# Performance work log

Hardware: AMD Instinct MI355X
Metric: run time of the kernel (lower is better)

## Reference

```python
import jax, jax.numpy as jnp
import numpy as np

DIM = 1024
N_HEADS = 16
HEAD_DIM = DIM // N_HEADS


def setup_inputs() -> dict:
    key = jax.random.key(0)
    ks = jax.random.split(key, 7)
    B, S = 2, 2048
    scale = 0.02
    return {
        "q": jax.random.normal(ks[0], (B, S, DIM), dtype=jnp.float32),
        "k": jax.random.normal(ks[1], (B, S, DIM), dtype=jnp.float32),
        "v": jax.random.normal(ks[2], (B, S, DIM), dtype=jnp.float32),
        # torch nn.Linear weights are [out_features, in_features]; y = x @ W.T
        "wq": jax.random.normal(ks[3], (DIM, DIM), dtype=jnp.float32) * scale,
        "wk": jax.random.normal(ks[4], (DIM, DIM), dtype=jnp.float32) * scale,
        "wv": jax.random.normal(ks[5], (DIM, DIM), dtype=jnp.float32) * scale,
        "wo": jax.random.normal(ks[6], (DIM, DIM), dtype=jnp.float32) * scale,
    }


def reference(q, k, v, wq, wk, wv, wo):
    B, S, _ = q.shape
    H, D = N_HEADS, HEAD_DIM
    # projections (torch Linear: x @ W.T), reshape to [B, H, S, D]
    xq = (q @ wq.T).reshape(B, S, H, D).transpose(0, 2, 1, 3)
    xk = (k @ wk.T).reshape(B, S, H, D).transpose(0, 2, 1, 3)
    xv = (v @ wv.T).reshape(B, S, H, D).transpose(0, 2, 1, 3)
    # scaled dot-product attention with causal mask
    scores = jnp.einsum("bhqd,bhkd->bhqk", xq, xk) / jnp.sqrt(jnp.float32(D))
    causal = jnp.tril(jnp.ones((S, S), dtype=bool))
    scores = jnp.where(causal, scores, -jnp.inf)
    attn = jax.nn.softmax(scores.astype(jnp.float32), axis=-1).astype(xq.dtype)
    # dropout prob = 0.0 (eval-mode / deterministic reference)
    out = jnp.einsum("bhqk,bhkd->bhqd", attn, xv)
    out = out.transpose(0, 2, 1, 3).reshape(B, S, H * D)
    return out @ wo.T
```

## Files before the change

kernel.cpp:

```cpp
#include <hip/hip_runtime.h>
#include <hip/hip_bf16.h>
#include <stdint.h>


typedef short s16x8 __attribute__((ext_vector_type(8)));
typedef float f32x4 __attribute__((ext_vector_type(4)));

#define MFMA_BF16 __builtin_amdgcn_mfma_f32_16x16x32_bf16

static __device__ __forceinline__ unsigned short f2bf(float f) {
    union { float f; unsigned u; } x{f};
    unsigned r = x.u + 0x7fff + ((x.u >> 16) & 1);
    return (unsigned short)(r >> 16);
}
static __device__ __forceinline__ unsigned pk2h(float a, float b) {
    __hip_bfloat162 h = __float22bfloat162_rn(float2{a, b});
    return *(unsigned*)&h;
}

static __device__ __forceinline__ void ald16(unsigned short* lds, const unsigned short* g) {
    __builtin_amdgcn_global_load_lds(
        (const __attribute__((address_space(1))) unsigned int*)g,
        (__attribute__((address_space(3))) unsigned int*)lds, 16, 0, 0);
}

#define QSCL 0.18033688f

__global__ __launch_bounds__(256) void convert_all_kernel(
        const float* __restrict__ q, const float* __restrict__ k,
        const float* __restrict__ v,
        const float* __restrict__ wq, const float* __restrict__ wk,
        const float* __restrict__ wv, const float* __restrict__ wo,
        unsigned short* __restrict__ dst) {
    const size_t idx = ((size_t)blockIdx.x * 256 + threadIdx.x) * 8;
    const int region = (int)(idx >> 22);
    const float* src;
    size_t off;
    if (region == 0)      { src = q; off = idx; }
    else if (region == 1) { src = k; off = idx & 4194303; }
    else if (region == 2) { src = v; off = idx & 4194303; }
    else {
        const int wsel = (int)((idx >> 20) & 3);
        src = wsel == 0 ? wq : wsel == 1 ? wk : wsel == 2 ? wv : wo;
        off = idx & 1048575;
    }
    const float4* p = (const float4*)(src + off);
    float4 a = p[0], b = p[1];
    uint4 u;
    u.x = pk2h(a.x, a.y); u.y = pk2h(a.z, a.w);
    u.z = pk2h(b.x, b.y); u.w = pk2h(b.z, b.w);
    *(uint4*)(dst + idx) = u;
}

__global__ __launch_bounds__(256) void wconvert_kernel(
        const float* __restrict__ wq, const float* __restrict__ wk,
        const float* __restrict__ wv, const float* __restrict__ wo,
        unsigned short* __restrict__ Wb) {
    const size_t idx = ((size_t)blockIdx.x * 256 + threadIdx.x) * 8;
    const int region = (int)(idx >> 20);
    const size_t off = idx & 1048575;
    const float* src = region == 0 ? wq : region == 1 ? wk : region == 2 ? wv : wo;
    const float4* p = (const float4*)(src + off);
    float4 a = p[0], b = p[1];
    uint4 u;
    u.x = pk2h(a.x, a.y); u.y = pk2h(a.z, a.w);
    u.z = pk2h(b.x, b.y); u.w = pk2h(b.z, b.w);
    *(uint4*)(Wb + idx) = u;
}

__global__ __launch_bounds__(256) void proj3b_kernel(
        const unsigned short* __restrict__ Qb, const unsigned short* __restrict__ Kb,
        const unsigned short* __restrict__ Vb, const unsigned short* __restrict__ Wb,
        unsigned short* __restrict__ Xq, unsigned short* __restrict__ Xk,
        unsigned short* __restrict__ Xvt) {
    constexpr int Kd = 1024;
    __shared__ union {
        struct { unsigned short A[128 * 32]; unsigned short B[128 * 32]; } s;
        unsigned short T[4 * 64 * 68];
    } sm;

    const int z = blockIdx.z;
    const unsigned short* A  = z == 0 ? Qb : z == 1 ? Kb : Vb;
    const unsigned short* Bw = Wb + (size_t)z * 1048576;

    const int t = threadIdx.x;
    const int m0 = blockIdx.x * 128, n0 = blockIdx.y * 128;
    const int w = t >> 6, lane = t & 63, fr = lane & 15, g = lane >> 4;
    const int wm = (w >> 1) * 64, wn = (w & 1) * 64;
    const int brow = t >> 2;
    const int cB = (t & 3) ^ ((t >> 3) & 3);
    const int sB = g ^ ((fr >> 1) & 3);

    f32x4 acc[4][4] = {};

    for (int k0 = 0; k0 < Kd; k0 += 32) {
        ald16(sm.s.A + (size_t)w * 512,        A  + (size_t)(m0 + brow) * Kd + k0 + cB * 8);
        ald16(sm.s.A + 2048 + (size_t)w * 512, A  + (size_t)(m0 + 64 + brow) * Kd + k0 + cB * 8);
        ald16(sm.s.B + (size_t)w * 512,        Bw + (size_t)(n0 + brow) * Kd + k0 + cB * 8);
        ald16(sm.s.B + 2048 + (size_t)w * 512, Bw + (size_t)(n0 + 64 + brow) * Kd + k0 + cB * 8);
        __syncthreads();

        s16x8 af[4], bfv[4];
#pragma unroll
        for (int mi = 0; mi < 4; ++mi)
            af[mi] = *(const s16x8*)(sm.s.A + (wm + mi * 16 + fr) * 32 + sB * 8);
#pragma unroll
        for (int ni = 0; ni < 4; ++ni)
            bfv[ni] = *(const s16x8*)(sm.s.B + (wn + ni * 16 + fr) * 32 + sB * 8);
#pragma unroll
        for (int mi = 0; mi < 4; ++mi)
#pragma unroll
            for (int ni = 0; ni < 4; ++ni)
                acc[mi][ni] = MFMA_BF16(af[mi], bfv[ni], acc[mi][ni], 0, 0, 0);
        __syncthreads();
    }

    if (z != 2) {
        unsigned short* C = z ? Xk : Xq;
        const float osc = z == 0 ? QSCL : 1.0f;
#pragma unroll
        for (int mi = 0; mi < 4; ++mi)
#pragma unroll
            for (int ni = 0; ni < 4; ++ni)
#pragma unroll
                for (int reg = 0; reg < 4; ++reg)
                    C[(size_t)(m0 + wm + mi * 16 + g * 4 + reg) * 1024 +
                      n0 + wn + ni * 16 + fr] = f2bf(acc[mi][ni][reg] * osc);
    } else {
        unsigned short* T = sm.T + w * (64 * 68);
#pragma unroll
        for (int mi = 0; mi < 4; ++mi)
#pragma unroll
            for (int ni = 0; ni < 4; ++ni) {
                uint2 u;
                u.x = pk2h(acc[mi][ni][0], acc[mi][ni][1]);
                u.y = pk2h(acc[mi][ni][2], acc[mi][ni][3]);
                *(uint2*)(T + (ni * 16 + fr) * 68 + mi * 16 + g * 4) = u;
            }
        __asm__ __volatile__("" ::: "memory");
#pragma unroll
        for (int pass = 0; pass < 8; ++pass) {
            const int row = pass * 8 + (lane >> 3);
            const int chk = lane & 7;
            uint4 d = *(const uint4*)(T + row * 68 + chk * 8);
            *(uint4*)(Xvt + (size_t)(n0 + wn + row) * 4096 + m0 + wm + chk * 8) = d;
        }
    }
}

__global__ __launch_bounds__(256) void proj3_kernel(
        const float* __restrict__ q, const float* __restrict__ k, const float* __restrict__ v,
        const unsigned short* __restrict__ Wb,
        unsigned short* __restrict__ Xq, unsigned short* __restrict__ Xk,
        unsigned short* __restrict__ Xvt) {
    constexpr int Kd = 1024;
    __shared__ unsigned short lsA[128 * 40];
    __shared__ unsigned short lsB[128 * 32];
    __shared__ unsigned short Tls[4 * 64 * 68];

    const int z = blockIdx.z;
    const float* A = z == 0 ? q : z == 1 ? k : v;
    const unsigned short* Bw = Wb + (size_t)z * 1048576;

    const int t = threadIdx.x;
    const int m0 = blockIdx.x * 128, n0 = blockIdx.y * 128;
    const int w = t >> 6, lane = t & 63, fr = lane & 15, g = lane >> 4, fq = g * 8;
    const int wm = (w >> 1) * 64, wn = (w & 1) * 64;
    const int ar = t >> 1, ac = (t & 1) * 16;
    const int brow = t >> 2;
    const int cB = (t & 3) ^ ((t >> 3) & 3);
    const int sB = g ^ ((fr >> 1) & 3);

    f32x4 acc[4][4] = {};

    for (int k0 = 0; k0 < Kd; k0 += 32) {
        ald16(lsB + (size_t)w * 512,        Bw + (size_t)(n0 + brow) * Kd + k0 + cB * 8);
        ald16(lsB + 2048 + (size_t)w * 512, Bw + (size_t)(n0 + 64 + brow) * Kd + k0 + cB * 8);
        {
            const float4* pa = (const float4*)(A + (size_t)(m0 + ar) * Kd + k0 + ac);
            float4 a0 = pa[0], a1 = pa[1], a2 = pa[2], a3 = pa[3];
            uint4 u0, u1;
            u0.x = pk2h(a0.x, a0.y); u0.y = pk2h(a0.z, a0.w);
            u0.z = pk2h(a1.x, a1.y); u0.w = pk2h(a1.z, a1.w);
            u1.x = pk2h(a2.x, a2.y); u1.y = pk2h(a2.z, a2.w);
            u1.z = pk2h(a3.x, a3.y); u1.w = pk2h(a3.z, a3.w);
            *(uint4*)(lsA + ar * 40 + ac)     = u0;
            *(uint4*)(lsA + ar * 40 + ac + 8) = u1;
        }
        __syncthreads();

        s16x8 af[4], bfv[4];
#pragma unroll
        for (int mi = 0; mi < 4; ++mi)
            af[mi] = *(const s16x8*)(lsA + (wm + mi * 16 + fr) * 40 + fq);
#pragma unroll
        for (int ni = 0; ni < 4; ++ni)
            bfv[ni] = *(const s16x8*)(lsB + (wn + ni * 16 + fr) * 32 + sB * 8);
#pragma unroll
        for (int mi = 0; mi < 4; ++mi)
#pragma unroll
            for (int ni = 0; ni < 4; ++ni)
                acc[mi][ni] = MFMA_BF16(af[mi], bfv[ni], acc[mi][ni], 0, 0, 0);
        __syncthreads();
    }

    if (z != 2) {
        unsigned short* C = z ? Xk : Xq;
        const float osc = z == 0 ? QSCL : 1.0f;
#pragma unroll
        for (int mi = 0; mi < 4; ++mi)
#pragma unroll
            for (int ni = 0; ni < 4; ++ni)
#pragma unroll
                for (int reg = 0; reg < 4; ++reg)
                    C[(size_t)(m0 + wm + mi * 16 + g * 4 + reg) * 1024 +
                      n0 + wn + ni * 16 + fr] = f2bf(acc[mi][ni][reg] * osc);
    } else {
        unsigned short* T = Tls + w * (64 * 68);
#pragma unroll
        for (int mi = 0; mi < 4; ++mi)
#pragma unroll
            for (int ni = 0; ni < 4; ++ni) {
                uint2 u;
                u.x = pk2h(acc[mi][ni][0], acc[mi][ni][1]);
                u.y = pk2h(acc[mi][ni][2], acc[mi][ni][3]);
                *(uint2*)(T + (ni * 16 + fr) * 68 + mi * 16 + g * 4) = u;
            }
        __asm__ __volatile__("" ::: "memory");
#pragma unroll
        for (int pass = 0; pass < 8; ++pass) {
            const int row = pass * 8 + (lane >> 3);
            const int chk = lane & 7;
            uint4 d = *(const uint4*)(T + row * 68 + chk * 8);
            *(uint4*)(Xvt + (size_t)(n0 + wn + row) * 4096 + m0 + wm + chk * 8) = d;
        }
    }
}

static __device__ __forceinline__ void slab_tail(
        const f32x4 sf[4], int kt, int qt, int qrow, float& l_part,
        f32x4* oacc, unsigned short* Pw, const s16x8 vf[4][2], int fr, int g) {
    float e[4][4];
    const bool diag = (kt == qt);
#pragma unroll
    for (int m16 = 0; m16 < 4; ++m16)
#pragma unroll
        for (int r = 0; r < 4; ++r) {
            float x = sf[m16][r];
            if (diag) {
                const int keyg = kt * 64 + m16 * 16 + g * 4 + r;
                x = (keyg <= qrow) ? x : -1e30f;
            }
            const float ee = exp2f(x);
            e[m16][r] = ee;
            l_part += ee;
        }
#pragma unroll
    for (int m16 = 0; m16 < 4; ++m16) {
        uint2 u;
        u.x = pk2h(e[m16][0], e[m16][1]);
        u.y = pk2h(e[m16][2], e[m16][3]);
        const int ch = 2 * m16 + (g >> 1);
        *(uint2*)(Pw + fr * 64 + ((ch ^ (fr & 7)) * 8) + (g & 1) * 4) = u;
    }
    __asm__ __volatile__("" ::: "memory");
    s16x8 pf0 = *(const s16x8*)(Pw + fr * 64 + ((g ^ (fr & 7)) * 8));
    s16x8 pf1 = *(const s16x8*)(Pw + fr * 64 + (((4 + g) ^ (fr & 7)) * 8));
#pragma unroll
    for (int m16 = 0; m16 < 4; ++m16) {
        oacc[m16] = MFMA_BF16(vf[m16][0], pf0, oacc[m16], 0, 0, 0);
        oacc[m16] = MFMA_BF16(vf[m16][1], pf1, oacc[m16], 0, 0, 0);
    }
    __asm__ __volatile__("" ::: "memory");
}

__global__ __launch_bounds__(256, 2) void flash_attn_kernel(
        const unsigned short* __restrict__ Xq, const unsigned short* __restrict__ Xk,
        const unsigned short* __restrict__ Xvt, unsigned short* __restrict__ Oa) {
    __shared__ unsigned short Kls[64 * 64];
    __shared__ unsigned short Vls[64 * 64];
    __shared__ unsigned short Pls[4][16 * 64];

    const int t = threadIdx.x;
    const int bh = blockIdx.x;
    const int j = blockIdx.y;
    const int b = bh >> 4, h = bh & 15;
    const size_t rbase = (size_t)b * 2048;
    const int cbase = h * 64;

    const int w = t >> 6, lane = t & 63, fr = lane & 15, g = lane >> 4, fq = g * 8;
    const int qtH = 31 - j, qtL = j;
    const int qrowH = qtH * 64 + w * 16 + fr;
    const int qrowL = qtL * 64 + w * 16 + fr;

    const unsigned short* qpH = Xq + (rbase + qrowH) * 1024 + cbase;
    s16x8 qfH0 = *(const s16x8*)(qpH + fq);
    s16x8 qfH1 = *(const s16x8*)(qpH + 32 + fq);
    const unsigned short* qpL = Xq + (rbase + qrowL) * 1024 + cbase;
    s16x8 qfL0 = *(const s16x8*)(qpL + fq);
    s16x8 qfL1 = *(const s16x8*)(qpL + 32 + fq);

    float lH = 0.f, lL = 0.f;
    f32x4 oH[4] = {}, oL[4] = {};

    const int r0 = w * 16 + (lane >> 3), r1 = r0 + 8;
    const int s8 = lane & 7;
    const int c0 = s8 ^ (r0 & 7), c1 = s8 ^ (r1 & 7);
    const unsigned short* kbase = Xk + rbase * 1024 + cbase;
    const size_t vrow0 = (size_t)(cbase + r0) * 4096 + rbase + c0 * 8;
    const size_t vrow1 = (size_t)(cbase + r1) * 4096 + rbase + c1 * 8;

    uint4 kA, kB, vA, vB;
    kA = *(const uint4*)(kbase + (size_t)r0 * 1024 + c0 * 8);
    kB = *(const uint4*)(kbase + (size_t)r1 * 1024 + c1 * 8);
    vA = *(const uint4*)(Xvt + vrow0);
    vB = *(const uint4*)(Xvt + vrow1);

    for (int kt = 0; kt <= qtH; ++kt) {
        *(uint4*)(Kls + (w * 16) * 64 + lane * 8)     = kA;
        *(uint4*)(Kls + (w * 16 + 8) * 64 + lane * 8) = kB;
        *(uint4*)(Vls + (w * 16) * 64 + lane * 8)     = vA;
        *(uint4*)(Vls + (w * 16 + 8) * 64 + lane * 8) = vB;
        __syncthreads();

        if (kt < qtH) {
            const unsigned short* ks = kbase + (size_t)(kt + 1) * 65536;
            kA = *(const uint4*)(ks + (size_t)r0 * 1024 + c0 * 8);
            kB = *(const uint4*)(ks + (size_t)r1 * 1024 + c1 * 8);
            vA = *(const uint4*)(Xvt + vrow0 + (size_t)(kt + 1) * 64);
            vB = *(const uint4*)(Xvt + vrow1 + (size_t)(kt + 1) * 64);
        }

        const bool doL = (kt <= qtL);

        s16x8 kf[4][2], vf[4][2];
#pragma unroll
        for (int m16 = 0; m16 < 4; ++m16) {
            const int rr = m16 * 16 + fr;
            kf[m16][0] = *(const s16x8*)(Kls + rr * 64 + ((g ^ (fr & 7)) * 8));
            kf[m16][1] = *(const s16x8*)(Kls + rr * 64 + (((4 + g) ^ (fr & 7)) * 8));
            vf[m16][0] = *(const s16x8*)(Vls + rr * 64 + ((g ^ (fr & 7)) * 8));
            vf[m16][1] = *(const s16x8*)(Vls + rr * 64 + (((4 + g) ^ (fr & 7)) * 8));
        }

        f32x4 sH[4], sL[4];
#pragma unroll
        for (int m16 = 0; m16 < 4; ++m16) {
            f32x4 zz = {};
            zz = MFMA_BF16(kf[m16][0], qfH0, zz, 0, 0, 0);
            sH[m16] = MFMA_BF16(kf[m16][1], qfH1, zz, 0, 0, 0);
        }
        if (doL) {
#pragma unroll
            for (int m16 = 0; m16 < 4; ++m16) {
                f32x4 zz = {};
                zz = MFMA_BF16(kf[m16][0], qfL0, zz, 0, 0, 0);
                sL[m16] = MFMA_BF16(kf[m16][1], qfL1, zz, 0, 0, 0);
            }
        }
        slab_tail(sH, kt, qtH, qrowH, lH, oH, &Pls[w][0], vf, fr, g);
        if (doL)
            slab_tail(sL, kt, qtL, qrowL, lL, oL, &Pls[w][0], vf, fr, g);
        __syncthreads();
    }

    lH += __shfl_xor(lH, 16, 64);
    lH += __shfl_xor(lH, 32, 64);
    lL += __shfl_xor(lL, 16, 64);
    lL += __shfl_xor(lL, 32, 64);
    const float invH = 1.0f / lH, invL = 1.0f / lL;
#pragma unroll
    for (int m16 = 0; m16 < 4; ++m16) {
        uint2 u;
        u.x = pk2h(oH[m16][0] * invH, oH[m16][1] * invH);
        u.y = pk2h(oH[m16][2] * invH, oH[m16][3] * invH);
        *(uint2*)(Oa + (rbase + qrowH) * 1024 + cbase + m16 * 16 + g * 4) = u;
        uint2 u2;
        u2.x = pk2h(oL[m16][0] * invL, oL[m16][1] * invL);
        u2.y = pk2h(oL[m16][2] * invL, oL[m16][3] * invL);
        *(uint2*)(Oa + (rbase + qrowL) * 1024 + cbase + m16 * 16 + g * 4) = u2;
    }
}

__global__ __launch_bounds__(256) void outproj_kernel(
        const unsigned short* __restrict__ Oa, const unsigned short* __restrict__ Wo,
        float* __restrict__ out) {
    constexpr int Kd = 1024;
    __shared__ unsigned short lsA[64 * 32];
    __shared__ unsigned short lsB[128 * 32];

    const int t = threadIdx.x;
    const int m0 = blockIdx.x * 64, n0 = blockIdx.y * 128;
    const int w = t >> 6, lane = t & 63, fr = lane & 15, g = lane >> 4;
    const int wm = (w >> 1) * 32, wn = (w & 1) * 64;
    const int brow = t >> 2;
    const int cB = (t & 3) ^ ((t >> 3) & 3);
    const int sB = g ^ ((fr >> 1) & 3);

    f32x4 acc[2][4] = {};

    for (int k0 = 0; k0 < Kd; k0 += 32) {
        ald16(lsA + (size_t)w * 512,        Oa + (size_t)(m0 + brow) * Kd + k0 + cB * 8);
        ald16(lsB + (size_t)w * 512,        Wo + (size_t)(n0 + brow) * Kd + k0 + cB * 8);
        ald16(lsB + 2048 + (size_t)w * 512, Wo + (size_t)(n0 + 64 + brow) * Kd + k0 + cB * 8);
        __syncthreads();

        s16x8 af[2], bfv[4];
#pragma unroll
        for (int mi = 0; mi < 2; ++mi)
            af[mi] = *(const s16x8*)(lsA + (wm + mi * 16 + fr) * 32 + sB * 8);
#pragma unroll
        for (int ni = 0; ni < 4; ++ni)
            bfv[ni] = *(const s16x8*)(lsB + (wn + ni * 16 + fr) * 32 + sB * 8);
#pragma unroll
        for (int mi = 0; mi < 2; ++mi)
#pragma unroll
            for (int ni = 0; ni < 4; ++ni)
                acc[mi][ni] = MFMA_BF16(af[mi], bfv[ni], acc[mi][ni], 0, 0, 0);
        __syncthreads();
    }

#pragma unroll
    for (int mi = 0; mi < 2; ++mi)
#pragma unroll
        for (int ni = 0; ni < 4; ++ni)
#pragma unroll
            for (int reg = 0; reg < 4; ++reg)
                out[(size_t)(m0 + wm + mi * 16 + g * 4 + reg) * 1024 +
                    n0 + wn + ni * 16 + fr] = acc[mi][ni][reg];
}

extern "C" void kernel_launch(void* const* d_in, const int* in_sizes, int n_in,
                              void* d_out, int out_size, void* d_ws, size_t ws_size,
                              hipStream_t stream) {
    const float* q  = (const float*)d_in[0];
    const float* k  = (const float*)d_in[1];
    const float* v  = (const float*)d_in[2];
    const float* wq = (const float*)d_in[3];
    const float* wk = (const float*)d_in[4];
    const float* wv = (const float*)d_in[5];
    const float* wo = (const float*)d_in[6];
    float* out = (float*)d_out;

    if (ws_size >= (size_t)64 * 1024 * 1024) {
        unsigned short* base = (unsigned short*)d_ws;
        unsigned short* Qb  = base;
        unsigned short* Kb  = base + 4194304;
        unsigned short* Vb  = base + 8388608;
        unsigned short* Wb  = base + 12582912;
        unsigned short* Xq  = base + 16777216;
        unsigned short* Xk  = base + 20971520;
        unsigned short* Xvt = base + 25165824;
        unsigned short* Oa  = base + 29360128;

        convert_all_kernel<<<8192, 256, 0, stream>>>(q, k, v, wq, wk, wv, wo, base);
        proj3b_kernel<<<dim3(32, 8, 3), 256, 0, stream>>>(Qb, Kb, Vb, Wb, Xq, Xk, Xvt);
        flash_attn_kernel<<<dim3(32, 16), 256, 0, stream>>>(Xq, Xk, Xvt, Oa);
        outproj_kernel<<<dim3(64, 8), 256, 0, stream>>>(Oa, Wb + 3145728, out);
    } else {
        unsigned short* Wb  = (unsigned short*)d_ws;
        unsigned short* Xq  = Wb  + 4194304;
        unsigned short* Xk  = Xq  + 4194304;
        unsigned short* Xvt = Xk  + 4194304;
        unsigned short* Oa  = Xvt + 4194304;

        wconvert_kernel<<<2048, 256, 0, stream>>>(wq, wk, wv, wo, Wb);
        proj3_kernel<<<dim3(32, 8, 3), 256, 0, stream>>>(q, k, v, Wb, Xq, Xk, Xvt);
        flash_attn_kernel<<<dim3(32, 16), 256, 0, stream>>>(Xq, Xk, Xvt, Oa);
        outproj_kernel<<<dim3(64, 8), 256, 0, stream>>>(Oa, Wb + 3145728, out);
    }
}
```

Baseline: 211.6 us.

## Triple-buffer LDS tiles with async prefetch in projection and output GEMMs

Result: faster. 201.9 us (-4.6%).

```diff
diff --git a/kernel.cpp b/kernel.cpp
--- a/kernel.cpp
+++ b/kernel.cpp
@@ -75,7 +75,7 @@
         unsigned short* __restrict__ Xvt) {
     constexpr int Kd = 1024;
     __shared__ union {
-        struct { unsigned short A[128 * 32]; unsigned short B[128 * 32]; } s;
+        struct { unsigned short A[3][128 * 32]; unsigned short B[3][128 * 32]; } s;
         unsigned short T[4 * 64 * 68];
     } sm;
 
@@ -93,26 +93,46 @@
 
     f32x4 acc[4][4] = {};
 
+    auto STAGE = [&](int p, int kk) {
+        ald16(sm.s.A[p] + (size_t)w * 512,        A  + (size_t)(m0 + brow) * Kd + kk + cB * 8);
+        ald16(sm.s.A[p] + 2048 + (size_t)w * 512, A  + (size_t)(m0 + 64 + brow) * Kd + kk + cB * 8);
+        ald16(sm.s.B[p] + (size_t)w * 512,        Bw + (size_t)(n0 + brow) * Kd + kk + cB * 8);
+        ald16(sm.s.B[p] + 2048 + (size_t)w * 512, Bw + (size_t)(n0 + 64 + brow) * Kd + kk + cB * 8);
+    };
+
+    STAGE(0, 0);
+    STAGE(1, 32);
+    int bi = 0, nb = 2;
+
     for (int k0 = 0; k0 < Kd; k0 += 32) {
-        ald16(sm.s.A + (size_t)w * 512,        A  + (size_t)(m0 + brow) * Kd + k0 + cB * 8);
-        ald16(sm.s.A + 2048 + (size_t)w * 512, A  + (size_t)(m0 + 64 + brow) * Kd + k0 + cB * 8);
-        ald16(sm.s.B + (size_t)w * 512,        Bw + (size_t)(n0 + brow) * Kd + k0 + cB * 8);
-        ald16(sm.s.B + 2048 + (size_t)w * 512, Bw + (size_t)(n0 + 64 + brow) * Kd + k0 + cB * 8);
-        __syncthreads();
+        if (k0 < Kd - 64) {
+            STAGE(nb, k0 + 64);
+            asm volatile("s_waitcnt vmcnt(8)" ::: "memory");
+        } else if (k0 < Kd - 32) {
+            asm volatile("s_waitcnt vmcnt(4)" ::: "memory");
+        } else {
+            asm volatile("s_waitcnt vmcnt(0)" ::: "memory");
+        }
+        __builtin_amdgcn_s_barrier();
+        asm volatile("" ::: "memory");
 
         s16x8 af[4], bfv[4];
 #pragma unroll
         for (int mi = 0; mi < 4; ++mi)
-            af[mi] = *(const s16x8*)(sm.s.A + (wm + mi * 16 + fr) * 32 + sB * 8);
+            af[mi] = *(const s16x8*)(sm.s.A[bi] + (wm + mi * 16 + fr) * 32 + sB * 8);
 #pragma unroll
         for (int ni = 0; ni < 4; ++ni)
-            bfv[ni] = *(const s16x8*)(sm.s.B + (wn + ni * 16 + fr) * 32 + sB * 8);
+            bfv[ni] = *(const s16x8*)(sm.s.B[bi] + (wn + ni * 16 + fr) * 32 + sB * 8);
 #pragma unroll
         for (int mi = 0; mi < 4; ++mi)
 #pragma unroll
             for (int ni = 0; ni < 4; ++ni)
                 acc[mi][ni] = MFMA_BF16(af[mi], bfv[ni], acc[mi][ni], 0, 0, 0);
-        __syncthreads();
+
+        asm volatile("" ::: "memory");
+        __builtin_amdgcn_s_barrier();
+        bi = bi == 2 ? 0 : bi + 1;
+        nb = nb == 2 ? 0 : nb + 1;
     }
 
     if (z != 2) {
@@ -386,8 +406,8 @@
         const unsigned short* __restrict__ Oa, const unsigned short* __restrict__ Wo,
         float* __restrict__ out) {
     constexpr int Kd = 1024;
-    __shared__ unsigned short lsA[64 * 32];
-    __shared__ unsigned short lsB[128 * 32];
+    __shared__ unsigned short lsA[3][64 * 32];
+    __shared__ unsigned short lsB[3][128 * 32];
 
     const int t = threadIdx.x;
     const int m0 = blockIdx.x * 64, n0 = blockIdx.y * 128;
@@ -399,25 +419,45 @@
 
     f32x4 acc[2][4] = {};
 
+    auto STAGE = [&](int p, int kk) {
+        ald16(lsA[p] + (size_t)w * 512,        Oa + (size_t)(m0 + brow) * Kd + kk + cB * 8);
+        ald16(lsB[p] + (size_t)w * 512,        Wo + (size_t)(n0 + brow) * Kd + kk + cB * 8);
+        ald16(lsB[p] + 2048 + (size_t)w * 512, Wo + (size_t)(n0 + 64 + brow) * Kd + kk + cB * 8);
+    };
+
+    STAGE(0, 0);
+    STAGE(1, 32);
+    int bi = 0, nb = 2;
+
     for (int k0 = 0; k0 < Kd; k0 += 32) {
-        ald16(lsA + (size_t)w * 512,        Oa + (size_t)(m0 + brow) * Kd + k0 + cB * 8);
-        ald16(lsB + (size_t)w * 512,        Wo + (size_t)(n0 + brow) * Kd + k0 + cB * 8);
-        ald16(lsB + 2048 + (size_t)w * 512, Wo + (size_t)(n0 + 64 + brow) * Kd + k0 + cB * 8);
-        __syncthreads();
+        if (k0 < Kd - 64) {
+            STAGE(nb, k0 + 64);
+            asm volatile("s_waitcnt vmcnt(6)" ::: "memory");
+        } else if (k0 < Kd - 32) {
+            asm volatile("s_waitcnt vmcnt(3)" ::: "memory");
+        } else {
+            asm volatile("s_waitcnt vmcnt(0)" ::: "memory");
+        }
+        __builtin_amdgcn_s_barrier();
+        asm volatile("" ::: "memory");
 
         s16x8 af[2], bfv[4];
 #pragma unroll
         for (int mi = 0; mi < 2; ++mi)
-            af[mi] = *(const s16x8*)(lsA + (wm + mi * 16 + fr) * 32 + sB * 8);
+            af[mi] = *(const s16x8*)(lsA[bi] + (wm + mi * 16 + fr) * 32 + sB * 8);
 #pragma unroll
         for (int ni = 0; ni < 4; ++ni)
-            bfv[ni] = *(const s16x8*)(lsB + (wn + ni * 16 + fr) * 32 + sB * 8);
+            bfv[ni] = *(const s16x8*)(lsB[bi] + (wn + ni * 16 + fr) * 32 + sB * 8);
 #pragma unroll
         for (int mi = 0; mi < 2; ++mi)
 #pragma unroll
             for (int ni = 0; ni < 4; ++ni)
                 acc[mi][ni] = MFMA_BF16(af[mi], bfv[ni], acc[mi][ni], 0, 0, 0);
-        __syncthreads();
+
+        asm volatile("" ::: "memory");
+        __builtin_amdgcn_s_barrier();
+        bi = bi == 2 ? 0 : bi + 1;
+        nb = nb == 2 ? 0 : nb + 1;
     }
 
 #pragma unroll
```
